# Performance work log

Hardware: AMD Instinct MI355X
Metric: run time of the kernel (lower is better)

## Reference

```python
import jax, jax.numpy as jnp
import numpy as np

TRANSLATE_STD = 0.125
SCALE_STD = 0.2
CUTOUT_SIZE = 0.5

B, C, H, W = 64, 3, 512, 512


def setup_inputs() -> dict:
    key = jax.random.key(0)
    ks = jax.random.split(key, 20)
    inp = {
        'images': jax.random.normal(ks[0], (B, C, H, W), dtype=jnp.float32),
        'u_angle': jax.random.uniform(ks[1], (B,), dtype=jnp.float32),
        'u_scale': jax.random.uniform(ks[2], (B,), dtype=jnp.float32),
        'u_trans': jax.random.uniform(ks[3], (B,), dtype=jnp.float32),
        'u_bright': jax.random.uniform(ks[4], (B,), dtype=jnp.float32),
        'u_contrast': jax.random.uniform(ks[5], (B,), dtype=jnp.float32),
        'u_sat': jax.random.uniform(ks[6], (B,), dtype=jnp.float32),
        'noise': jax.random.normal(ks[7], (B, C, H, W), dtype=jnp.float32),
        'm_flip': jax.random.randint(ks[8], (B,), 0, 2, dtype=jnp.int32),
        'm_rot': jax.random.randint(ks[9], (B,), 0, 2, dtype=jnp.int32),
        'm_scale': jax.random.randint(ks[10], (B,), 0, 2, dtype=jnp.int32),
        'm_trans': jax.random.randint(ks[11], (B,), 0, 2, dtype=jnp.int32),
        'm_bright': jax.random.randint(ks[12], (B,), 0, 2, dtype=jnp.int32),
        'm_contrast': jax.random.randint(ks[13], (B,), 0, 2, dtype=jnp.int32),
        'm_sat': jax.random.randint(ks[14], (B,), 0, 2, dtype=jnp.int32),
        'm_cut': jax.random.randint(ks[15], (B,), 0, 2, dtype=jnp.int32),
        'y0': jax.random.randint(ks[16], (B,), 0, H - int(H * CUTOUT_SIZE) + 1, dtype=jnp.int32),
        'x0': jax.random.randint(ks[17], (B,), 0, W - int(W * CUTOUT_SIZE) + 1, dtype=jnp.int32),
    }
    return inp


def _sample_bilinear_reflect(img, gx, gy):
    # img: [C,H,W]; gx, gy: [H,W] normalized coords in grid_sample convention
    # (align_corners=False, padding_mode='reflection')
    c, h, w = img.shape
    x = ((gx + 1.0) * w - 1.0) * 0.5
    y = ((gy + 1.0) * h - 1.0) * 0.5

    def reflect(v, size):
        # reflect about pixel edges [-0.5, size-0.5], then clip coordinate
        v = jnp.abs(v + 0.5)
        v = jnp.mod(v, 2.0 * size)
        v = jnp.minimum(v, 2.0 * size - v)
        return jnp.clip(v - 0.5, 0.0, size - 1.0)

    x = reflect(x, float(w))
    y = reflect(y, float(h))
    x0f = jnp.floor(x)
    y0f = jnp.floor(y)
    wx = x - x0f
    wy = y - y0f
    x0i = jnp.clip(x0f, 0, w - 1).astype(jnp.int32)
    x1i = jnp.clip(x0f + 1, 0, w - 1).astype(jnp.int32)
    y0i = jnp.clip(y0f, 0, h - 1).astype(jnp.int32)
    y1i = jnp.clip(y0f + 1, 0, h - 1).astype(jnp.int32)
    v00 = img[:, y0i, x0i]
    v01 = img[:, y0i, x1i]
    v10 = img[:, y1i, x0i]
    v11 = img[:, y1i, x1i]
    top = v00 + wx * (v01 - v00)
    bot = v10 + wx * (v11 - v10)
    return top + wy * (bot - top)


def reference(images, u_angle, u_scale, u_trans, u_bright, u_contrast, u_sat,
              noise, m_flip, m_rot, m_scale, m_trans, m_bright, m_contrast,
              m_sat, m_cut, y0, x0):
    b, c, h, w = images.shape
    # xflip
    images = jnp.where((m_flip > 0)[:, None, None, None], images[..., ::-1], images)
    # rotate / scale / translate (single value broadcast to both axes, as in original)
    angle = jnp.where(m_rot > 0, (u_angle * 2.0 - 1.0) * jnp.pi, 0.0)
    sc = jnp.where(m_scale > 0, (u_scale * 2.0 - 1.0) * SCALE_STD + 1.0, 1.0)
    tr = jnp.where(m_trans > 0, (u_trans * 2.0 - 1.0) * TRANSLATE_STD, 0.0)
    ca = jnp.cos(angle)[:, None, None]
    sa = jnp.sin(angle)[:, None, None]
    scb = sc[:, None, None]
    trb = tr[:, None, None]
    gx0, gy0 = jnp.meshgrid(jnp.linspace(-1.0, 1.0, w), jnp.linspace(-1.0, 1.0, h), indexing='xy')  # [H,W]
    gx = scb * (ca * gx0 - sa * gy0) + trb  # [B,H,W]
    gy = scb * (sa * gx0 + ca * gy0) + trb
    images = jax.vmap(_sample_bilinear_reflect)(images, gx, gy)
    # brightness
    bb = jnp.where(m_bright > 0, u_bright * 0.2, 0.0)
    images = jnp.clip(images + bb[:, None, None, None], -1.0, 1.0)
    # contrast
    cc = jnp.where(m_contrast > 0, u_contrast + 0.5, 1.0)
    images = jnp.clip(images * cc[:, None, None, None], -1.0, 1.0)
    # saturation: lerp(grayscale, images, s)
    ss = jnp.where(m_sat > 0, u_sat * 2.0, 1.0)[:, None, None, None]
    gray = images.mean(axis=1, keepdims=True)
    images = jnp.clip(gray + ss * (images - gray), -1.0, 1.0)
    ch, cw = int(h * CUTOUT_SIZE), int(w * CUTOUT_SIZE)
    ys = jnp.arange(h)[None, :, None]
    xs = jnp.arange(w)[None, None, :]
    y0b = y0[:, None, None]
    x0b = x0[:, None, None]
    cmask = (ys >= y0b) & (ys < y0b + ch) & (xs >= x0b) & (xs < x0b + cw)
    fmask = cmask & (m_cut > 0)[:, None, None]
    images = jnp.where(fmask[:, None, :, :], noise, images)
    return images
```

## Files before the change

kernel.cpp:

```cpp
#include <hip/hip_runtime.h>
#include <math.h>


constexpr int Bn = 64;
constexpr int Cn = 3;
constexpr int Hn = 512;
constexpr int Wn = 512;
constexpr float TRANSLATE_STD = 0.125f;
constexpr float SCALE_STD = 0.2f;
constexpr int CUT_H = 256;
constexpr int CUT_W = 256;

constexpr int FW = 32;
constexpr int FSTRIDE = 40;
constexpr int FH_MAX = 32;
constexpr int CH_LDS = FSTRIDE * FH_MAX;
constexpr int NT = 8;
constexpr uint32_t PLANE = 512u * 512u;

typedef float f4v __attribute__((ext_vector_type(4)));

__device__ __forceinline__ int refl(int v) {
    v = (v < 0) ? (-1 - v) : v;
    return (v > 511) ? (1023 - v) : v;
}

__device__ __forceinline__ void pipe_barrier() {
    asm volatile("s_waitcnt lgkmcnt(0)" ::: "memory");
    __builtin_amdgcn_s_barrier();
    __builtin_amdgcn_sched_barrier(0);
}

__global__ __launch_bounds__(256) void augment_kernel(
    const float* __restrict__ images,
    const float* __restrict__ u_angle,
    const float* __restrict__ u_scale,
    const float* __restrict__ u_trans,
    const float* __restrict__ u_bright,
    const float* __restrict__ u_contrast,
    const float* __restrict__ u_sat,
    const float* __restrict__ noise,
    const int* __restrict__ m_flip,
    const int* __restrict__ m_rot,
    const int* __restrict__ m_scale,
    const int* __restrict__ m_trans,
    const int* __restrict__ m_bright,
    const int* __restrict__ m_contrast,
    const int* __restrict__ m_sat,
    const int* __restrict__ m_cut,
    const int* __restrict__ y0p,
    const int* __restrict__ x0p,
    float* __restrict__ out)
{
    __shared__ __align__(16) float lds[Cn * CH_LDS];

    const int lin = blockIdx.x + (blockIdx.y << 2) + (blockIdx.z << 7);
    const int swz = ((lin & 7) << 10) + (lin >> 3);
    const int sx0 = (swz & 3) << 7;
    const int y16 = (swz >> 2) & 31;
    const int b   = swz >> 7;

    const int tx  = threadIdx.x;
    const int ty  = threadIdx.y;
    const int y   = (y16 << 4) + ty;

    const float angle = (m_rot[b] > 0) ? (u_angle[b] * 2.0f - 1.0f) * 3.14159265358979323846f : 0.0f;
    const float sc    = (m_scale[b] > 0) ? (u_scale[b] * 2.0f - 1.0f) * SCALE_STD + 1.0f : 1.0f;
    const float tr    = (m_trans[b] > 0) ? (u_trans[b] * 2.0f - 1.0f) * TRANSLATE_STD : 0.0f;
    const float bb    = (m_bright[b] > 0) ? u_bright[b] * 0.2f : 0.0f;
    const float cc    = (m_contrast[b] > 0) ? u_contrast[b] + 0.5f : 1.0f;
    const float ss    = (m_sat[b] > 0) ? u_sat[b] * 2.0f : 1.0f;
    const bool  flip  = m_flip[b] > 0;
    const bool  docut = m_cut[b] > 0;
    const int   cy0   = y0p[b];
    const int   cx0   = x0p[b];

    float saf, caf;
    __sincosf(angle, &saf, &caf);

    const float kk = sc * (512.0f / 511.0f);
    const float dxdx = caf * kk, dxdy = -saf * kk;
    const float dydx = saf * kk, dydy = caf * kk;
    const float xx_org = 256.0f * (sc * (saf - caf) + tr + 1.0f) - 0.5f;
    const float yy_org = 256.0f * (sc * (-saf - caf) + tr + 1.0f) - 0.5f;

    const float step_x = 16.0f * dxdx;
    const float step_y = 16.0f * dydx;

    float xxt = xx_org + (float)(sx0 + tx) * dxdx + (float)y * dxdy;
    float yyt = yy_org + (float)(sx0 + tx) * dydx + (float)y * dydy;

    const float fty = (float)(y16 << 4);
    float bx = xx_org + (float)sx0 * dxdx + fty * dxdy;
    float by = yy_org + (float)sx0 * dydx + fty * dydy;
    const float sxx = 15.0f * dxdx, sxy = 15.0f * dxdy;
    const float syx = 15.0f * dydx, syy = 15.0f * dydy;
    const float min_dx = fminf(sxx, 0.0f) + fminf(sxy, 0.0f);
    const float min_dy = fminf(syx, 0.0f) + fminf(syy, 0.0f);
    const float max_dy = fmaxf(syx, 0.0f) + fmaxf(syy, 0.0f);

    const float* __restrict__ imgb = images + (size_t)b * (Cn * PLANE);
    float* __restrict__ outb       = out    + (size_t)b * (Cn * PLANE);
    const float* __restrict__ noib = noise  + (size_t)b * (Cn * PLANE);

    const int tid = ty * 16 + tx;
    const int sr  = tid >> 3;
    const int sq  = (tid & 7) << 2;

    const bool ycut = docut && (y >= cy0) && (y < cy0 + CUT_H);
    uint32_t opix = (uint32_t)y * 512u + (uint32_t)(sx0 + tx);

    int cx_lo, cy_lo, cfh;
    int nx_lo, ny_lo, nfh;
    auto mkbox = [&](float bxv, float byv, int& x_lo, int& y_lo, int& fh) {
        x_lo = (int)floorf(bxv + min_dx) - 1;
        y_lo = (int)floorf(byv + min_dy) - 1;
        fh   = min(((int)floorf(byv + max_dy) + 2) - y_lo + 1, FH_MAX);
    };

    f4v A{}, B{}, C{};
    bool rev = false;
    auto loadR = [&](int x_lo, int y_lo) {
        const uint32_t ro = (uint32_t)refl(y_lo + sr) * 512u;
        const int c0 = x_lo + sq;
        int S0 = refl(c0);     if (flip) S0 = 511 - S0;
        int S3 = refl(c0 + 3); if (flip) S3 = 511 - S3;
        const int d = S3 - S0;
        if (d == 3) {
            rev = false;
            __builtin_memcpy(&A, imgb + ro + S0, 16);
            __builtin_memcpy(&B, imgb + ro + S0 + PLANE, 16);
            __builtin_memcpy(&C, imgb + ro + S0 + 2 * PLANE, 16);
        } else if (d == -3) {
            rev = true;
            __builtin_memcpy(&A, imgb + ro + S3, 16);
            __builtin_memcpy(&B, imgb + ro + S3 + PLANE, 16);
            __builtin_memcpy(&C, imgb + ro + S3 + 2 * PLANE, 16);
        } else {
            rev = false;
            int S1 = refl(c0 + 1); if (flip) S1 = 511 - S1;
            int S2 = refl(c0 + 2); if (flip) S2 = 511 - S2;
            A = f4v{imgb[ro + S0], imgb[ro + S1], imgb[ro + S2], imgb[ro + S3]};
            const float* p1 = imgb + PLANE;
            B = f4v{p1[ro + S0], p1[ro + S1], p1[ro + S2], p1[ro + S3]};
            const float* p2 = imgb + 2 * PLANE;
            C = f4v{p2[ro + S0], p2[ro + S1], p2[ro + S2], p2[ro + S3]};
        }
    };
    auto writeR = [&]() {
        f4v a = A, b2 = B, c2 = C;
        if (rev) {
            a  = f4v{A.w, A.z, A.y, A.x};
            b2 = f4v{B.w, B.z, B.y, B.x};
            c2 = f4v{C.w, C.z, C.y, C.x};
        }
        float* d = &lds[sr * FSTRIDE + sq];
        *(f4v*)(d)              = a;
        *(f4v*)(d + CH_LDS)     = b2;
        *(f4v*)(d + 2 * CH_LDS) = c2;
    };

    mkbox(bx, by, cx_lo, cy_lo, cfh);
    if (sr < cfh) { loadR(cx_lo, cy_lo); writeR(); }
    bx += step_x; by += step_y;
    mkbox(bx, by, nx_lo, ny_lo, nfh);
    if (sr < nfh) loadR(nx_lo, ny_lo);
    pipe_barrier();

    #pragma unroll 1
    for (int t = 0; t < NT; ++t) {
        const float fx = xxt - (float)cx_lo;
        const float fy = yyt - (float)cy_lo;
        const int xi = (int)fx;
        const int yi = (int)fy;
        const float wx = fx - (float)xi;
        const float wy = fy - (float)yi;
        const float* ph = &lds[yi * FSTRIDE + xi];

        float vals[Cn];
        #pragma unroll
        for (int c = 0; c < Cn; ++c) {
            const float v00 = ph[0], v01 = ph[1];
            const float v10 = ph[FSTRIDE], v11 = ph[FSTRIDE + 1];
            ph += CH_LDS;
            const float top = v00 + wx * (v01 - v00);
            const float bot = v10 + wx * (v11 - v10);
            float v = top + wy * (bot - top);
            v = __builtin_amdgcn_fmed3f(v + bb, -1.0f, 1.0f);
            v = __builtin_amdgcn_fmed3f(v * cc, -1.0f, 1.0f);
            vals[c] = v;
        }

        const float gray = (vals[0] + vals[1] + vals[2]) * (1.0f / 3.0f);
        const int xpix = sx0 + (t << 4) + tx;
        const bool cut = ycut && (xpix >= cx0) && (xpix < cx0 + CUT_W);
        #pragma unroll
        for (int c = 0; c < Cn; ++c) {
            float v = gray + ss * (vals[c] - gray);
            v = __builtin_amdgcn_fmed3f(v, -1.0f, 1.0f);
            if (cut) v = noib[opix + c * PLANE];
            outb[opix + c * PLANE] = v;
        }
        opix += 16;
        xxt += step_x; yyt += step_y;

        if (t == NT - 1) break;

        pipe_barrier();
        cx_lo = nx_lo; cy_lo = ny_lo; cfh = nfh;
        if (sr < cfh) writeR();
        bx += step_x; by += step_y;
        if (t + 2 < NT) {
            mkbox(bx, by, nx_lo, ny_lo, nfh);
            if (sr < nfh) loadR(nx_lo, ny_lo);
        } else {
            nfh = 0;
        }
        pipe_barrier();
    }
}

extern "C" void kernel_launch(void* const* d_in, const int* in_sizes, int n_in,
                              void* d_out, int out_size, void* d_ws, size_t ws_size,
                              hipStream_t stream) {
    const float* images     = (const float*)d_in[0];
    const float* u_angle    = (const float*)d_in[1];
    const float* u_scale    = (const float*)d_in[2];
    const float* u_trans    = (const float*)d_in[3];
    const float* u_bright   = (const float*)d_in[4];
    const float* u_contrast = (const float*)d_in[5];
    const float* u_sat      = (const float*)d_in[6];
    const float* noise      = (const float*)d_in[7];
    const int*   m_flip     = (const int*)d_in[8];
    const int*   m_rot      = (const int*)d_in[9];
    const int*   m_scale    = (const int*)d_in[10];
    const int*   m_trans    = (const int*)d_in[11];
    const int*   m_bright   = (const int*)d_in[12];
    const int*   m_contrast = (const int*)d_in[13];
    const int*   m_sat      = (const int*)d_in[14];
    const int*   m_cut      = (const int*)d_in[15];
    const int*   y0p        = (const int*)d_in[16];
    const int*   x0p        = (const int*)d_in[17];
    float* out = (float*)d_out;

    dim3 block(16, 16);
    dim3 grid(Wn / (16 * NT), Hn / 16, Bn);
    augment_kernel<<<grid, block, 0, stream>>>(
        images, u_angle, u_scale, u_trans, u_bright, u_contrast, u_sat, noise,
        m_flip, m_rot, m_scale, m_trans, m_bright, m_contrast, m_sat, m_cut,
        y0p, x0p, out);
}
```

Before: 526.0 us.

## Give each wavefront a private LDS footprint and drop block barriers

Restructures the kernel so each 64-lane wavefront handles its own 8x8 output tile and stages a private 20x16 source footprint per channel in its own LDS slice. Because a wavefront executes in order, no block-wide barriers are needed, and the load/write/compute software pipeline runs per wave. The grid is re-swizzled to 1D 256-thread blocks with 16 horizontal steps, and launch bounds now request higher occupancy. The risk is that the fixed 16-row, 20-column footprint may be too small for the larger scale/rotation cases. The per-tile 1-column extra load also adds some redundant global traffic.

```diff
diff --git a/kernel.cpp b/kernel.cpp
--- a/kernel.cpp
+++ b/kernel.cpp
@@ -11,11 +11,12 @@
 constexpr int CUT_H = 256;
 constexpr int CUT_W = 256;
 
-constexpr int FW = 32;
-constexpr int FSTRIDE = 40;
-constexpr int FH_MAX = 32;
-constexpr int CH_LDS = FSTRIDE * FH_MAX;
-constexpr int NT = 8;
+constexpr int FW = 20;
+constexpr int FH = 16;
+constexpr int FSTR = 20;
+constexpr int SLICE = FSTR * FH;
+constexpr int WSLICE = Cn * SLICE;
+constexpr int NT = 16;
 constexpr uint32_t PLANE = 512u * 512u;
 
 typedef float f4v __attribute__((ext_vector_type(4)));
@@ -25,13 +26,7 @@
     return (v > 511) ? (1023 - v) : v;
 }
 
-__device__ __forceinline__ void pipe_barrier() {
-    asm volatile("s_waitcnt lgkmcnt(0)" ::: "memory");
-    __builtin_amdgcn_s_barrier();
-    __builtin_amdgcn_sched_barrier(0);
-}
-
-__global__ __launch_bounds__(256) void augment_kernel(
+__global__ __launch_bounds__(256, 8) void augment_kernel(
     const float* __restrict__ images,
     const float* __restrict__ u_angle,
     const float* __restrict__ u_scale,
@@ -52,17 +47,23 @@
     const int* __restrict__ x0p,
     float* __restrict__ out)
 {
-    __shared__ __align__(16) float lds[Cn * CH_LDS];
-
-    const int lin = blockIdx.x + (blockIdx.y << 2) + (blockIdx.z << 7);
-    const int swz = ((lin & 7) << 10) + (lin >> 3);
-    const int sx0 = (swz & 3) << 7;
-    const int y16 = (swz >> 2) & 31;
-    const int b   = swz >> 7;
-
-    const int tx  = threadIdx.x;
-    const int ty  = threadIdx.y;
-    const int y   = (y16 << 4) + ty;
+    __shared__ __align__(16) float lds[4 * WSLICE];
+
+    const int tid  = threadIdx.x;
+    const int wid  = tid >> 6;
+    const int lane = tid & 63;
+    const int lx   = lane & 7;
+    const int ly   = lane >> 3;
+    const int srow = lane >> 2;
+    const int sq   = (lane & 3) << 2;
+    const int sqe  = 16 + (lane & 3);
+
+    const int lin  = blockIdx.x + (blockIdx.y << 6);
+    const int loc  = lin >> 3;
+    const int b    = ((lin & 7) << 3) + (loc >> 6);
+    const int band = loc & 63;
+
+    const int y = (band << 3) + ly;
 
     const float angle = (m_rot[b] > 0) ? (u_angle[b] * 2.0f - 1.0f) * 3.14159265358979323846f : 0.0f;
     const float sc    = (m_scale[b] > 0) ? (u_scale[b] * 2.0f - 1.0f) * SCALE_STD + 1.0f : 1.0f;
@@ -84,105 +85,118 @@
     const float xx_org = 256.0f * (sc * (saf - caf) + tr + 1.0f) - 0.5f;
     const float yy_org = 256.0f * (sc * (-saf - caf) + tr + 1.0f) - 0.5f;
 
-    const float step_x = 16.0f * dxdx;
-    const float step_y = 16.0f * dydx;
-
-    float xxt = xx_org + (float)(sx0 + tx) * dxdx + (float)y * dxdy;
-    float yyt = yy_org + (float)(sx0 + tx) * dydx + (float)y * dydy;
-
-    const float fty = (float)(y16 << 4);
-    float bx = xx_org + (float)sx0 * dxdx + fty * dxdy;
-    float by = yy_org + (float)sx0 * dydx + fty * dydy;
-    const float sxx = 15.0f * dxdx, sxy = 15.0f * dxdy;
-    const float syx = 15.0f * dydx, syy = 15.0f * dydy;
+    const float step_x = 32.0f * dxdx;
+    const float step_y = 32.0f * dydx;
+
+    const float w8 = (float)(wid << 3);
+    const float b8 = (float)(band << 3);
+
+    float xxt = xx_org + (w8 + (float)lx) * dxdx + (float)y * dxdy;
+    float yyt = yy_org + (w8 + (float)lx) * dydx + (float)y * dydy;
+
+    float bx = xx_org + w8 * dxdx + b8 * dxdy;
+    float by = yy_org + w8 * dydx + b8 * dydy;
+    const float sxx = 7.0f * dxdx, sxy = 7.0f * dxdy;
+    const float syx = 7.0f * dydx, syy = 7.0f * dydy;
     const float min_dx = fminf(sxx, 0.0f) + fminf(sxy, 0.0f);
     const float min_dy = fminf(syx, 0.0f) + fminf(syy, 0.0f);
-    const float max_dy = fmaxf(syx, 0.0f) + fmaxf(syy, 0.0f);
 
     const float* __restrict__ imgb = images + (size_t)b * (Cn * PLANE);
     float* __restrict__ outb       = out    + (size_t)b * (Cn * PLANE);
     const float* __restrict__ noib = noise  + (size_t)b * (Cn * PLANE);
 
-    const int tid = ty * 16 + tx;
-    const int sr  = tid >> 3;
-    const int sq  = (tid & 7) << 2;
+    float* const wbase = lds + wid * WSLICE;
 
     const bool ycut = docut && (y >= cy0) && (y < cy0 + CUT_H);
-    uint32_t opix = (uint32_t)y * 512u + (uint32_t)(sx0 + tx);
-
-    int cx_lo, cy_lo, cfh;
-    int nx_lo, ny_lo, nfh;
-    auto mkbox = [&](float bxv, float byv, int& x_lo, int& y_lo, int& fh) {
-        x_lo = (int)floorf(bxv + min_dx) - 1;
-        y_lo = (int)floorf(byv + min_dy) - 1;
-        fh   = min(((int)floorf(byv + max_dy) + 2) - y_lo + 1, FH_MAX);
+    uint32_t opix = (uint32_t)y * 512u + (uint32_t)((wid << 3) + lx);
+
+    int x_lo, y_lo, nx_lo, ny_lo;
+    auto mkbox = [&](float bxv, float byv, int& xl, int& yl) {
+        xl = (((int)floorf(bxv + min_dx)) - 1) & ~3;
+        yl = ((int)floorf(byv + min_dy)) - 1;
     };
 
-    f4v A{}, B{}, C{};
+    f4v A{}, Bq{}, Cq{};
+    float Ae = 0.f, Be = 0.f, Ce = 0.f;
     bool rev = false;
-    auto loadR = [&](int x_lo, int y_lo) {
-        const uint32_t ro = (uint32_t)refl(y_lo + sr) * 512u;
-        const int c0 = x_lo + sq;
+
+    auto loadR = [&](int xl, int yl) {
+        const uint32_t ro = (uint32_t)refl(yl + srow) * 512u;
+        const int c0 = xl + sq;
         int S0 = refl(c0);     if (flip) S0 = 511 - S0;
         int S3 = refl(c0 + 3); if (flip) S3 = 511 - S3;
         const int d = S3 - S0;
         if (d == 3) {
             rev = false;
-            __builtin_memcpy(&A, imgb + ro + S0, 16);
-            __builtin_memcpy(&B, imgb + ro + S0 + PLANE, 16);
-            __builtin_memcpy(&C, imgb + ro + S0 + 2 * PLANE, 16);
+            __builtin_memcpy(&A,  imgb + ro + S0, 16);
+            __builtin_memcpy(&Bq, imgb + ro + S0 + PLANE, 16);
+            __builtin_memcpy(&Cq, imgb + ro + S0 + 2 * PLANE, 16);
         } else if (d == -3) {
             rev = true;
-            __builtin_memcpy(&A, imgb + ro + S3, 16);
-            __builtin_memcpy(&B, imgb + ro + S3 + PLANE, 16);
-            __builtin_memcpy(&C, imgb + ro + S3 + 2 * PLANE, 16);
+            __builtin_memcpy(&A,  imgb + ro + S3, 16);
+            __builtin_memcpy(&Bq, imgb + ro + S3 + PLANE, 16);
+            __builtin_memcpy(&Cq, imgb + ro + S3 + 2 * PLANE, 16);
         } else {
             rev = false;
             int S1 = refl(c0 + 1); if (flip) S1 = 511 - S1;
             int S2 = refl(c0 + 2); if (flip) S2 = 511 - S2;
-            A = f4v{imgb[ro + S0], imgb[ro + S1], imgb[ro + S2], imgb[ro + S3]};
+            A  = f4v{imgb[ro + S0], imgb[ro + S1], imgb[ro + S2], imgb[ro + S3]};
             const float* p1 = imgb + PLANE;
-            B = f4v{p1[ro + S0], p1[ro + S1], p1[ro + S2], p1[ro + S3]};
+            Bq = f4v{p1[ro + S0], p1[ro + S1], p1[ro + S2], p1[ro + S3]};
             const float* p2 = imgb + 2 * PLANE;
-            C = f4v{p2[ro + S0], p2[ro + S1], p2[ro + S2], p2[ro + S3]};
-        }
+            Cq = f4v{p2[ro + S0], p2[ro + S1], p2[ro + S2], p2[ro + S3]};
+        }
+        int Se = refl(xl + sqe); if (flip) Se = 511 - Se;
+        Ae = imgb[ro + Se];
+        Be = imgb[ro + Se + PLANE];
+        Ce = imgb[ro + Se + 2 * PLANE];
     };
+
     auto writeR = [&]() {
-        f4v a = A, b2 = B, c2 = C;
+        f4v a = A, b2 = Bq, c2 = Cq;
         if (rev) {
-            a  = f4v{A.w, A.z, A.y, A.x};
-            b2 = f4v{B.w, B.z, B.y, B.x};
-            c2 = f4v{C.w, C.z, C.y, C.x};
-        }
-        float* d = &lds[sr * FSTRIDE + sq];
-        *(f4v*)(d)              = a;
-        *(f4v*)(d + CH_LDS)     = b2;
-        *(f4v*)(d + 2 * CH_LDS) = c2;
+            a  = f4v{A.w,  A.z,  A.y,  A.x};
+            b2 = f4v{Bq.w, Bq.z, Bq.y, Bq.x};
+            c2 = f4v{Cq.w, Cq.z, Cq.y, Cq.x};
+        }
+        float* d0 = wbase + srow * FSTR + sq;
+        *(f4v*)(d0)             = a;
+        *(f4v*)(d0 + SLICE)     = b2;
+        *(f4v*)(d0 + 2 * SLICE) = c2;
+        float* de = wbase + srow * FSTR + sqe;
+        de[0]         = Ae;
+        de[SLICE]     = Be;
+        de[2 * SLICE] = Ce;
     };
 
-    mkbox(bx, by, cx_lo, cy_lo, cfh);
-    if (sr < cfh) { loadR(cx_lo, cy_lo); writeR(); }
-    bx += step_x; by += step_y;
-    mkbox(bx, by, nx_lo, ny_lo, nfh);
-    if (sr < nfh) loadR(nx_lo, ny_lo);
-    pipe_barrier();
+    mkbox(bx, by, x_lo, y_lo);
+    loadR(x_lo, y_lo);
 
     #pragma unroll 1
     for (int t = 0; t < NT; ++t) {
-        const float fx = xxt - (float)cx_lo;
-        const float fy = yyt - (float)cy_lo;
+        writeR();
+        const int cxl = x_lo, cyl = y_lo;
+        if (t + 1 < NT) {
+            bx += step_x; by += step_y;
+            mkbox(bx, by, nx_lo, ny_lo);
+            loadR(nx_lo, ny_lo);
+            x_lo = nx_lo; y_lo = ny_lo;
+        }
+
+        const float fx = xxt - (float)cxl;
+        const float fy = yyt - (float)cyl;
         const int xi = (int)fx;
         const int yi = (int)fy;
         const float wx = fx - (float)xi;
         const float wy = fy - (float)yi;
-        const float* ph = &lds[yi * FSTRIDE + xi];
+        const float* p = wbase + yi * FSTR + xi;
 
         float vals[Cn];
         #pragma unroll
         for (int c = 0; c < Cn; ++c) {
-            const float v00 = ph[0], v01 = ph[1];
-            const float v10 = ph[FSTRIDE], v11 = ph[FSTRIDE + 1];
-            ph += CH_LDS;
+            const float v00 = p[0], v01 = p[1];
+            const float v10 = p[FSTR], v11 = p[FSTR + 1];
+            p += SLICE;
             const float top = v00 + wx * (v01 - v00);
             const float bot = v10 + wx * (v11 - v10);
             float v = top + wy * (bot - top);
@@ -192,7 +206,7 @@
         }
 
         const float gray = (vals[0] + vals[1] + vals[2]) * (1.0f / 3.0f);
-        const int xpix = sx0 + (t << 4) + tx;
+        const int xpix = (wid << 3) + (t << 5) + lx;
         const bool cut = ycut && (xpix >= cx0) && (xpix < cx0 + CUT_W);
         #pragma unroll
         for (int c = 0; c < Cn; ++c) {
@@ -201,22 +215,8 @@
             if (cut) v = noib[opix + c * PLANE];
             outb[opix + c * PLANE] = v;
         }
-        opix += 16;
+        opix += 32;
         xxt += step_x; yyt += step_y;
-
-        if (t == NT - 1) break;
-
-        pipe_barrier();
-        cx_lo = nx_lo; cy_lo = ny_lo; cfh = nfh;
-        if (sr < cfh) writeR();
-        bx += step_x; by += step_y;
-        if (t + 2 < NT) {
-            mkbox(bx, by, nx_lo, ny_lo, nfh);
-            if (sr < nfh) loadR(nx_lo, ny_lo);
-        } else {
-            nfh = 0;
-        }
-        pipe_barrier();
     }
 }
 
@@ -243,8 +243,8 @@
     const int*   x0p        = (const int*)d_in[17];
     float* out = (float*)d_out;
 
-    dim3 block(16, 16);
-    dim3 grid(Wn / (16 * NT), Hn / 16, Bn);
+    dim3 block(256, 1, 1);
+    dim3 grid(64, 64, 1);
     augment_kernel<<<grid, block, 0, stream>>>(
         images, u_angle, u_scale, u_trans, u_bright, u_contrast, u_sat, noise,
         m_flip, m_rot, m_scale, m_trans, m_bright, m_contrast, m_sat, m_cut,
```

Measured after the change: 624.2 us. +18.7%, slower.
